# Optimization experiments

Measured on AMD Instinct MI355X. Metric: run time of the kernel, lower is better.

The kernel has to match this reference:

```python
import jax, jax.numpy as jnp
import numpy as np
import math

D_MODEL = 2048
NUM_HEADS = 16
HEAD_DIM = D_MODEL // NUM_HEADS  # 128
B, S = 2, 2048


def setup_inputs() -> dict:
    key = jax.random.key(0)
    ks = jax.random.split(key, 11)
    s_in = 1.0 / math.sqrt(D_MODEL)
    return {
        "query": jax.random.normal(ks[0], (B, S, D_MODEL), dtype=jnp.float32),
        "key": jax.random.normal(ks[1], (B, S, D_MODEL), dtype=jnp.float32),
        "value": jax.random.normal(ks[2], (B, S, D_MODEL), dtype=jnp.float32),
        "Wq": jax.random.normal(ks[3], (D_MODEL, D_MODEL), dtype=jnp.float32) * s_in,
        "bq": jnp.zeros((D_MODEL,), dtype=jnp.float32),
        "Wk": jax.random.normal(ks[4], (D_MODEL, HEAD_DIM), dtype=jnp.float32) * s_in,
        "bk": jnp.zeros((HEAD_DIM,), dtype=jnp.float32),
        "Wv": jax.random.normal(ks[5], (D_MODEL, HEAD_DIM), dtype=jnp.float32) * s_in,
        "bv": jnp.zeros((HEAD_DIM,), dtype=jnp.float32),
        "Wo": jax.random.normal(ks[6], (D_MODEL, D_MODEL), dtype=jnp.float32) * s_in,
        "bo": jnp.zeros((D_MODEL,), dtype=jnp.float32),
    }


def reference(query, key, value, Wq, bq, Wk, bk, Wv, bv, Wo, bo):
    b, s, d_model = query.shape
    h, d = NUM_HEADS, HEAD_DIM
    # Projections: Q has h heads, K/V have a single shared head (MQA)
    Q = (query @ Wq + bq).reshape(b, s, h, d).transpose(0, 2, 1, 3)  # [b,h,s,d]
    K = key @ Wk + bk      # [b,s,d]
    V = value @ Wv + bv    # [b,s,d]
    scale = 1.0 / math.sqrt(d)
    # broadcast single K head over all h query heads
    scores = jnp.einsum('bhqd,bkd->bhqk', Q, K) * scale  # [b,h,s,s]
    weights = jax.nn.softmax(scores, axis=-1)
    attn = jnp.einsum('bhqk,bkd->bhqd', weights, V)      # [b,h,s,d]
    attn = attn.transpose(0, 2, 1, 3).reshape(b, s, d_model)
    return attn @ Wo + bo
```

## Files before the change

kernel.cpp:

```cpp
#include <hip/hip_runtime.h>


typedef unsigned short u16;
typedef __attribute__((ext_vector_type(8))) short bf16x8;
typedef __attribute__((ext_vector_type(4))) short bf16x4;
typedef __attribute__((ext_vector_type(4))) float f32x4;

#define D_MODEL 2048
#define SEQ     2048
#define NH      16
#define HD      128
#define BK      32

__device__ __forceinline__ u16 f2bf(float f){
  union { float f; unsigned u; } v; v.f = f;
  unsigned r = (v.u + 0x7FFFu + ((v.u >> 16) & 1u)) >> 16;
  return (u16)r;
}

#if __has_builtin(__builtin_amdgcn_cvt_pk_bf16_f32)
__device__ __forceinline__ unsigned pack2bf(float a, float b){
  auto v = __builtin_amdgcn_cvt_pk_bf16_f32(a, b);
  unsigned u; __builtin_memcpy(&u, &v, 4); return u;
}
#else
__device__ __forceinline__ unsigned pack2bf(float a, float b){
  return (unsigned)f2bf(a) | ((unsigned)f2bf(b) << 16);
}
#endif

__device__ __forceinline__ void gll16(const void* g, void* l){
  __builtin_amdgcn_global_load_lds(
      (const __attribute__((address_space(1))) void*)g,
      (__attribute__((address_space(3))) void*)l, 16, 0, 0);
}

__global__ __launch_bounds__(256) void convert3_kernel(
    const float4* __restrict__ a, const float4* __restrict__ b, const float4* __restrict__ c,
    ushort4* __restrict__ oa, ushort4* __restrict__ ob, ushort4* __restrict__ oc){
  int i = blockIdx.x*256 + threadIdx.x;
  float4 va = a[i], vb = b[i], vc = c[i];
  ushort4 ra, rb, rc;
  ra.x=f2bf(va.x); ra.y=f2bf(va.y); ra.z=f2bf(va.z); ra.w=f2bf(va.w);
  rb.x=f2bf(vb.x); rb.y=f2bf(vb.y); rb.z=f2bf(vb.z); rb.w=f2bf(vb.w);
  rc.x=f2bf(vc.x); rc.y=f2bf(vc.y); rc.z=f2bf(vc.z); rc.w=f2bf(vc.w);
  oa[i]=ra; ob[i]=rb; oc[i]=rc;
}

__global__ __launch_bounds__(256) void transpose_all(
    const float* __restrict__ Wq, const float* __restrict__ Wo,
    const float* __restrict__ Wk, const float* __restrict__ Wv,
    u16* __restrict__ WqT, u16* __restrict__ WoT,
    u16* __restrict__ WkT, u16* __restrict__ WvT){
  __shared__ float tt[32][33];
  int id = blockIdx.x;
  const float* in; u16* outp; int C, bx, by;
  if (id < 4096)      { in=Wq; outp=WqT; C=2048; bx=id&63;        by=id>>6; }
  else if (id < 8192) { id-=4096; in=Wo; outp=WoT; C=2048; bx=id&63; by=id>>6; }
  else if (id < 8448) { id-=8192; in=Wk; outp=WkT; C=128;  bx=id&3;  by=id>>2; }
  else                { id-=8448; in=Wv; outp=WvT; C=128;  bx=id&3;  by=id>>2; }
  const int R = 2048;
  int c0 = bx*32, r0 = by*32;
  int tx = threadIdx.x & 31, ty = threadIdx.x >> 5;
  #pragma unroll
  for (int k=0;k<4;k++) tt[ty+k*8][tx] = in[(size_t)(r0+ty+k*8)*C + c0+tx];
  __syncthreads();
  #pragma unroll
  for (int k=0;k<4;k++) outp[(size_t)(c0+ty+k*8)*R + r0+tx] = f2bf(tt[tx][ty+k*8]);
}

__device__ __forceinline__ void gemm_core_db(
    const u16* __restrict__ A, const u16* __restrict__ BT,
    int lda, int ldb, int m0, int n0, int kbeg, int kend,
    u16* As, u16* Bs, f32x4 acc[4][4])
{
  const int t = threadIdx.x;
  const int w = t >> 6, l = t & 63;
  const int wr = w >> 1, wc = w & 1;
  const int c16 = l & 15, q = l >> 4;
  const int srow = l >> 2;
  const int sc   = ((l & 3) ^ ((l >> 3) & 3)) * 8;

  int aoff[4], boff[4];
  #pragma unroll
  for (int mt=0;mt<4;mt++){
    int row = wr*64 + mt*16 + c16;
    aoff[mt] = row*BK + ((q ^ ((row>>1)&3))*8);
  }
  #pragma unroll
  for (int nt=0;nt<4;nt++){
    int row = wc*64 + nt*16 + c16;
    boff[nt] = row*BK + ((q ^ ((row>>1)&3))*8);
  }

  auto issue = [&](int k0, int buf){
    u16* Ad = As + buf*4096;
    u16* Bd = Bs + buf*4096;
    #pragma unroll
    for (int half=0; half<2; half++){
      int r = half*64 + w*16 + srow;
      gll16(A  + (size_t)(m0+r)*lda + k0 + sc, Ad + (half*64 + w*16)*BK);
      gll16(BT + (size_t)(n0+r)*ldb + k0 + sc, Bd + (half*64 + w*16)*BK);
    }
  };

  const int n = (kend - kbeg) / BK;
  issue(kbeg, 0);
  for (int i = 0; i < n; i++){
    __syncthreads();
    if (i+1 < n) issue(kbeg + (i+1)*BK, (i+1)&1);
    const u16* Ab = As + (i&1)*4096;
    const u16* Bb = Bs + (i&1)*4096;
    bf16x8 af[4], bfr[4];
    #pragma unroll
    for (int mt=0;mt<4;mt++) af[mt]  = *(const bf16x8*)(Ab + aoff[mt]);
    #pragma unroll
    for (int nt=0;nt<4;nt++) bfr[nt] = *(const bf16x8*)(Bb + boff[nt]);
    #pragma unroll
    for (int mt=0;mt<4;mt++)
      #pragma unroll
      for (int nt=0;nt<4;nt++)
        acc[mt][nt] = __builtin_amdgcn_mfma_f32_16x16x32_bf16(af[mt], bfr[nt], acc[mt][nt], 0,0,0);
  }
}

__global__ __launch_bounds__(256) void proj_kernel(
    const u16* __restrict__ qb, const u16* __restrict__ kb, const u16* __restrict__ vb,
    const u16* __restrict__ WqT, const u16* __restrict__ WkT, const u16* __restrict__ WvT,
    const float* __restrict__ bq, u16* __restrict__ Qp, float* __restrict__ part)
{
  __shared__ u16 As[2*4096], Bs[2*4096];
  f32x4 acc[4][4];
  f32x4 z = {0.f,0.f,0.f,0.f};
  #pragma unroll
  for (int i=0;i<4;i++) for (int j=0;j<4;j++) acc[i][j] = z;
  const int t = threadIdx.x, w = t>>6, l = t&63, wr = w>>1, wc = w&1, c16 = l&15, q = l>>4;
  int id = blockIdx.x;
  if (id < 512){
    int m0 = (id & 31)*128, n0 = (id >> 5)*128;
    gemm_core_db(qb, WqT, 2048, 2048, m0, n0, 0, 2048, As, Bs, acc);
    #pragma unroll
    for (int mt=0;mt<4;mt++)
      #pragma unroll
      for (int nt=0;nt<4;nt++){
        int col = n0 + wc*64 + nt*16 + c16;
        float bv = bq[col];
        #pragma unroll
        for (int r=0;r<4;r++){
          int row = m0 + wr*64 + mt*16 + q*4 + r;
          Qp[(size_t)row*D_MODEL + col] = f2bf(acc[mt][nt][r] + bv);
        }
      }
  } else {
    int kvid = id - 512;
    int zi = kvid & 3, nb = (kvid >> 2) & 1, mi = kvid >> 3;
    const u16* Am = nb ? vb  : kb;
    const u16* Bm = nb ? WvT : WkT;
    gemm_core_db(Am, Bm, 2048, 2048, mi*128, 0, zi*512, zi*512+512, As, Bs, acc);
    float* dst = part + (size_t)(zi*2 + nb)*524288;
    #pragma unroll
    for (int mt=0;mt<4;mt++)
      #pragma unroll
      for (int nt=0;nt<4;nt++){
        int col = wc*64 + nt*16 + c16;
        #pragma unroll
        for (int r=0;r<4;r++){
          int row = mi*128 + wr*64 + mt*16 + q*4 + r;
          dst[(size_t)row*128 + col] = acc[mt][nt][r];
        }
      }
  }
}

__global__ __launch_bounds__(256) void oproj_kernel(
    const u16* __restrict__ A, const u16* __restrict__ BT, const float* __restrict__ bias,
    float* __restrict__ C)
{
  __shared__ u16 As[2*4096], Bs[2*4096];
  f32x4 acc[4][4];
  f32x4 z = {0.f,0.f,0.f,0.f};
  #pragma unroll
  for (int i=0;i<4;i++) for (int j=0;j<4;j++) acc[i][j] = z;
  int m0 = blockIdx.x*128, n0 = blockIdx.y*128;
  gemm_core_db(A, BT, 2048, 2048, m0, n0, 0, 2048, As, Bs, acc);
  const int t = threadIdx.x, w = t>>6, l = t&63, wr = w>>1, wc = w&1, c16 = l&15, q = l>>4;
  #pragma unroll
  for (int mt=0;mt<4;mt++)
    #pragma unroll
    for (int nt=0;nt<4;nt++){
      int col = n0 + wc*64 + nt*16 + c16;
      float bv = bias[col];
      #pragma unroll
      for (int r=0;r<4;r++){
        int row = m0 + wr*64 + mt*16 + q*4 + r;
        C[(size_t)row*D_MODEL + col] = acc[mt][nt][r] + bv;
      }
    }
}

__global__ __launch_bounds__(256) void kv_reduce_kernel(
    const float* __restrict__ part, const float* __restrict__ bk, const float* __restrict__ bv,
    u16* __restrict__ Kp, u16* __restrict__ VpT){
  int idx = blockIdx.x*256 + threadIdx.x;
  int d = idx & 127, sg = idx >> 7;
  float ka = 0.f, va = 0.f;
  #pragma unroll
  for (int zi=0; zi<4; zi++){
    ka += part[(size_t)(zi*2+0)*524288 + idx];
    va += part[(size_t)(zi*2+1)*524288 + idx];
  }
  Kp[idx] = f2bf(ka + bk[d]);
  int b = sg >> 11, sl = sg & 2047;
  VpT[(size_t)b*262144 + (size_t)d*2048 + sl] = f2bf(va + bv[d]);
}

__global__ __launch_bounds__(512, 2) void attn_kernel(
    const u16* __restrict__ Qp, const u16* __restrict__ Kp,
    const u16* __restrict__ VpT, u16* __restrict__ attnb){
  __shared__ u16 lds[65536];
  const int t = threadIdx.x;
  const int w = t >> 6, l = t & 63;
  const int c16 = l & 15, q = l >> 4;

  const int qt = blockIdx.x;
  const int bh = blockIdx.y;
  const int b = bh >> 4, h = bh & 15;

  const u16* Qbase = Qp  + ((size_t)(b*SEQ + qt*256 + w*32))*D_MODEL + h*HD;
  const u16* Kbase = Kp  + (size_t)(b*SEQ)*HD;
  const u16* Vbase = VpT + (size_t)b*HD*SEQ;

  const int sr = w*4 + (l >> 4);
  #pragma unroll
  for (int j=0;j<4;j++){
    int r = j*32 + sr;
    int g = (l & 15) ^ (r & 15);
    gll16(Kbase + (size_t)r*HD + g*8, lds + j*4096 + w*512);
  }
  #pragma unroll
  for (int j=0;j<4;j++){
    int d = j*32 + sr;
    int g = (l & 15) ^ (d & 15);
    gll16(Vbase + (size_t)d*SEQ + g*8, lds + 32768 + j*4096 + w*512);
  }
  bf16x8 qf[2][4];
  #pragma unroll
  for (int qs=0;qs<2;qs++)
    #pragma unroll
    for (int kk=0;kk<4;kk++)
      qf[qs][kk] = *(const bf16x8*)(Qbase + (size_t)(qs*16 + c16)*D_MODEL + (kk*4 + q)*8);
  __syncthreads();

  f32x4 o[2][8];
  f32x4 z4 = {0.f,0.f,0.f,0.f};
  #pragma unroll
  for (int qs=0;qs<2;qs++) for (int dt=0;dt<8;dt++) o[qs][dt] = z4;
  float mrow[2] = {-1e30f, -1e30f};
  float lrow[2] = {0.f, 0.f};
  const float cs = 0.08838834764831845f * 1.4426950408889634f;

  for (int kt = 0; kt < 16; kt++){
    const int p = kt & 1;
    if (kt < 15){
      u16* Kd = lds + (p^1)*16384;
      u16* Vd = lds + 32768 + (p^1)*16384;
      #pragma unroll
      for (int j=0;j<4;j++){
        int r = j*32 + sr;
        int g = (l & 15) ^ (r & 15);
        gll16(Kbase + (size_t)((kt+1)*128 + r)*HD + g*8, Kd + j*4096 + w*512);
      }
      #pragma unroll
      for (int j=0;j<4;j++){
        int d = j*32 + sr;
        int g = (l & 15) ^ (d & 15);
        gll16(Vbase + (size_t)d*SEQ + (kt+1)*128 + g*8, Vd + j*4096 + w*512);
      }
    }
    const u16* Ks = lds + p*16384;
    const u16* Vs = lds + 32768 + p*16384;

    f32x4 s[2][8];
    #pragma unroll
    for (int qs=0;qs<2;qs++) for (int kt8=0;kt8<8;kt8++) s[qs][kt8] = z4;
    __builtin_amdgcn_s_setprio(1);
    #pragma unroll
    for (int kt8=0; kt8<8; kt8++){
      #pragma unroll
      for (int kk=0;kk<4;kk++){
        int ch = kk*4 + q;
        bf16x8 kf = *(const bf16x8*)(Ks + (kt8*16 + c16)*128 + ((ch ^ c16) & 15)*8);
        s[0][kt8] = __builtin_amdgcn_mfma_f32_16x16x32_bf16(kf, qf[0][kk], s[0][kt8], 0,0,0);
        s[1][kt8] = __builtin_amdgcn_mfma_f32_16x16x32_bf16(kf, qf[1][kk], s[1][kt8], 0,0,0);
      }
    }
    __builtin_amdgcn_s_setprio(0);

    float alpha[2];
    #pragma unroll
    for (int qs=0; qs<2; qs++){
      float x[8];
      #pragma unroll
      for (int kt8=0;kt8<8;kt8++)
        x[kt8] = fmaxf(fmaxf(s[qs][kt8][0],s[qs][kt8][1]), fmaxf(s[qs][kt8][2],s[qs][kt8][3]));
      float vmax = fmaxf(fmaxf(fmaxf(x[0],x[1]),fmaxf(x[2],x[3])),
                         fmaxf(fmaxf(x[4],x[5]),fmaxf(x[6],x[7])));
      vmax = fmaxf(vmax, __shfl_xor(vmax, 16));
      vmax = fmaxf(vmax, __shfl_xor(vmax, 32));
      float mnew = fmaxf(mrow[qs], vmax);
      alpha[qs] = exp2f((mrow[qs] - mnew)*cs);
      float mc = mnew*cs;
      float rs[8];
      #pragma unroll
      for (int kt8=0;kt8<8;kt8++){
        float p0 = exp2f(__builtin_fmaf(s[qs][kt8][0], cs, -mc));
        float p1 = exp2f(__builtin_fmaf(s[qs][kt8][1], cs, -mc));
        float p2 = exp2f(__builtin_fmaf(s[qs][kt8][2], cs, -mc));
        float p3 = exp2f(__builtin_fmaf(s[qs][kt8][3], cs, -mc));
        s[qs][kt8][0]=p0; s[qs][kt8][1]=p1; s[qs][kt8][2]=p2; s[qs][kt8][3]=p3;
        rs[kt8] = (p0+p1)+(p2+p3);
      }
      float rsum = ((rs[0]+rs[1])+(rs[2]+rs[3])) + ((rs[4]+rs[5])+(rs[6]+rs[7]));
      rsum += __shfl_xor(rsum, 16);
      rsum += __shfl_xor(rsum, 32);
      lrow[qs] = lrow[qs]*alpha[qs] + rsum;
      mrow[qs] = mnew;
    }

    unsigned long long allone = __ballot(alpha[0] == 1.f && alpha[1] == 1.f);
    if (allone != ~0ull){
      #pragma unroll
      for (int qs=0;qs<2;qs++)
        #pragma unroll
        for (int dt=0;dt<8;dt++)
          #pragma unroll
          for (int r=0;r<4;r++) o[qs][dt][r] *= alpha[qs];
    }

    union PU { unsigned u[4]; bf16x8 v; } P32[2][4];
    #pragma unroll
    for (int qs=0;qs<2;qs++)
      #pragma unroll
      for (int kb=0;kb<4;kb++){
        P32[qs][kb].u[0] = pack2bf(s[qs][2*kb][0],   s[qs][2*kb][1]);
        P32[qs][kb].u[1] = pack2bf(s[qs][2*kb][2],   s[qs][2*kb][3]);
        P32[qs][kb].u[2] = pack2bf(s[qs][2*kb+1][0], s[qs][2*kb+1][1]);
        P32[qs][kb].u[3] = pack2bf(s[qs][2*kb+1][2], s[qs][2*kb+1][3]);
      }

    __builtin_amdgcn_s_setprio(1);
    #pragma unroll
    for (int kb=0; kb<4; kb++){
      int ca = 4*kb + (q>>1);
      int cb = ca + 2;
      #pragma unroll
      for (int dt=0; dt<8; dt++){
        int d = dt*16 + c16;
        union VU { bf16x4 h[2]; bf16x8 v; } vf;
        vf.h[0] = *(const bf16x4*)(Vs + d*128 + ((ca ^ c16) & 15)*8 + (q&1)*4);
        vf.h[1] = *(const bf16x4*)(Vs + d*128 + ((cb ^ c16) & 15)*8 + (q&1)*4);
        o[0][dt] = __builtin_amdgcn_mfma_f32_16x16x32_bf16(vf.v, P32[0][kb].v, o[0][dt], 0,0,0);
        o[1][dt] = __builtin_amdgcn_mfma_f32_16x16x32_bf16(vf.v, P32[1][kb].v, o[1][dt], 0,0,0);
      }
    }
    __builtin_amdgcn_s_setprio(0);
    __syncthreads();
  }

  #pragma unroll
  for (int qs=0;qs<2;qs++){
    float inv = 1.f / lrow[qs];
    int qrow = qt*256 + w*32 + qs*16 + c16;
    u16* dst = attnb + ((size_t)(b*SEQ) + qrow)*D_MODEL + h*HD + q*4;
    #pragma unroll
    for (int dt=0;dt<8;dt++){
      ushort4 pk;
      pk.x = f2bf(o[qs][dt][0]*inv);
      pk.y = f2bf(o[qs][dt][1]*inv);
      pk.z = f2bf(o[qs][dt][2]*inv);
      pk.w = f2bf(o[qs][dt][3]*inv);
      *(ushort4*)(dst + dt*16) = pk;
    }
  }
}

extern "C" void kernel_launch(void* const* d_in, const int* in_sizes, int n_in,
                              void* d_out, int out_size, void* d_ws, size_t ws_size,
                              hipStream_t stream) {
  (void)in_sizes; (void)n_in; (void)out_size; (void)ws_size;
  const float* query = (const float*)d_in[0];
  const float* key   = (const float*)d_in[1];
  const float* value = (const float*)d_in[2];
  const float* Wq    = (const float*)d_in[3];
  const float* bq    = (const float*)d_in[4];
  const float* Wk    = (const float*)d_in[5];
  const float* bk    = (const float*)d_in[6];
  const float* Wv    = (const float*)d_in[7];
  const float* bv    = (const float*)d_in[8];
  const float* Wo    = (const float*)d_in[9];
  const float* bo    = (const float*)d_in[10];
  float* out = (float*)d_out;

  char* W = (char*)d_ws;
  u16*  qb     = (u16*) (W + 0);
  u16*  kb     = (u16*) (W + 16777216);
  u16*  vb     = (u16*) (W + 33554432);
  u16*  WqT    = (u16*) (W + 50331648);
  u16*  WoT    = (u16*) (W + 58720256);
  u16*  WkT    = (u16*) (W + 67108864);
  u16*  WvT    = (u16*) (W + 67633152);
  u16*  Qp     = (u16*) (W + 68157440);
  u16*  Kp     = (u16*) (W + 84934656);
  u16*  VpT    = (u16*) (W + 85983232);
  u16*  attnb  = (u16*) (W + 87031808);
  float* kvpart= (float*)(W + 103809024);

  convert3_kernel<<<8192, 256, 0, stream>>>(
      (const float4*)query, (const float4*)key, (const float4*)value,
      (ushort4*)qb, (ushort4*)kb, (ushort4*)vb);
  transpose_all<<<8704, 256, 0, stream>>>(Wq, Wo, Wk, Wv, WqT, WoT, WkT, WvT);
  proj_kernel<<<768, 256, 0, stream>>>(qb, kb, vb, WqT, WkT, WvT, bq, Qp, kvpart);
  kv_reduce_kernel<<<2048, 256, 0, stream>>>(kvpart, bk, bv, Kp, VpT);
  attn_kernel<<<dim3(8,32), 512, 0, stream>>>(Qp, Kp, VpT, attnb);
  oproj_kernel<<<dim3(32,16), 256, 0, stream>>>(attnb, WoT, bo, out);
}
```

Baseline: 411.8 us.

## Split softmax into half-tiles with lazy max rescaling threshold

Splits each 128-key tile into two 64-key halves, each with its own max, exp, pack and PV MFMA phase. This lets softmax math for one half interleave with matrix work for the other. It also adds a lazy rescale: the running max and the output accumulator are updated only when some row's new max exceeds the old one by more than 8 in log2 units. Otherwise exponentials are computed against the stale max, which skips most rescale multiplies but risks larger intermediate values.

```diff
diff --git a/kernel.cpp b/kernel.cpp
--- a/kernel.cpp
+++ b/kernel.cpp
@@ -281,84 +281,175 @@
     const u16* Vs = lds + 32768 + p*16384;
 
     f32x4 s[2][8];
-    #pragma unroll
-    for (int qs=0;qs<2;qs++) for (int kt8=0;kt8<8;kt8++) s[qs][kt8] = z4;
+    union PU { unsigned u[4]; bf16x8 v; } P32[2][4];
+
     __builtin_amdgcn_s_setprio(1);
     #pragma unroll
-    for (int kt8=0; kt8<8; kt8++){
-      #pragma unroll
-      for (int kk=0;kk<4;kk++){
+    for (int kt8=0; kt8<4; kt8++){
+      {
+        bf16x8 kf = *(const bf16x8*)(Ks + (kt8*16 + c16)*128 + ((q ^ c16) & 15)*8);
+        s[0][kt8] = __builtin_amdgcn_mfma_f32_16x16x32_bf16(kf, qf[0][0], z4, 0,0,0);
+        s[1][kt8] = __builtin_amdgcn_mfma_f32_16x16x32_bf16(kf, qf[1][0], z4, 0,0,0);
+      }
+      #pragma unroll
+      for (int kk=1;kk<4;kk++){
         int ch = kk*4 + q;
         bf16x8 kf = *(const bf16x8*)(Ks + (kt8*16 + c16)*128 + ((ch ^ c16) & 15)*8);
         s[0][kt8] = __builtin_amdgcn_mfma_f32_16x16x32_bf16(kf, qf[0][kk], s[0][kt8], 0,0,0);
         s[1][kt8] = __builtin_amdgcn_mfma_f32_16x16x32_bf16(kf, qf[1][kk], s[1][kt8], 0,0,0);
       }
     }
+    #pragma unroll
+    for (int kt8=4; kt8<8; kt8++){
+      {
+        bf16x8 kf = *(const bf16x8*)(Ks + (kt8*16 + c16)*128 + ((q ^ c16) & 15)*8);
+        s[0][kt8] = __builtin_amdgcn_mfma_f32_16x16x32_bf16(kf, qf[0][0], z4, 0,0,0);
+        s[1][kt8] = __builtin_amdgcn_mfma_f32_16x16x32_bf16(kf, qf[1][0], z4, 0,0,0);
+      }
+      #pragma unroll
+      for (int kk=1;kk<4;kk++){
+        int ch = kk*4 + q;
+        bf16x8 kf = *(const bf16x8*)(Ks + (kt8*16 + c16)*128 + ((ch ^ c16) & 15)*8);
+        s[0][kt8] = __builtin_amdgcn_mfma_f32_16x16x32_bf16(kf, qf[0][kk], s[0][kt8], 0,0,0);
+        s[1][kt8] = __builtin_amdgcn_mfma_f32_16x16x32_bf16(kf, qf[1][kk], s[1][kt8], 0,0,0);
+      }
+    }
     __builtin_amdgcn_s_setprio(0);
 
-    float alpha[2];
-    #pragma unroll
-    for (int qs=0; qs<2; qs++){
-      float x[8];
-      #pragma unroll
-      for (int kt8=0;kt8<8;kt8++)
-        x[kt8] = fmaxf(fmaxf(s[qs][kt8][0],s[qs][kt8][1]), fmaxf(s[qs][kt8][2],s[qs][kt8][3]));
-      float vmax = fmaxf(fmaxf(fmaxf(x[0],x[1]),fmaxf(x[2],x[3])),
-                         fmaxf(fmaxf(x[4],x[5]),fmaxf(x[6],x[7])));
-      vmax = fmaxf(vmax, __shfl_xor(vmax, 16));
-      vmax = fmaxf(vmax, __shfl_xor(vmax, 32));
-      float mnew = fmaxf(mrow[qs], vmax);
-      alpha[qs] = exp2f((mrow[qs] - mnew)*cs);
-      float mc = mnew*cs;
-      float rs[8];
-      #pragma unroll
-      for (int kt8=0;kt8<8;kt8++){
-        float p0 = exp2f(__builtin_fmaf(s[qs][kt8][0], cs, -mc));
-        float p1 = exp2f(__builtin_fmaf(s[qs][kt8][1], cs, -mc));
-        float p2 = exp2f(__builtin_fmaf(s[qs][kt8][2], cs, -mc));
-        float p3 = exp2f(__builtin_fmaf(s[qs][kt8][3], cs, -mc));
-        s[qs][kt8][0]=p0; s[qs][kt8][1]=p1; s[qs][kt8][2]=p2; s[qs][kt8][3]=p3;
-        rs[kt8] = (p0+p1)+(p2+p3);
-      }
-      float rsum = ((rs[0]+rs[1])+(rs[2]+rs[3])) + ((rs[4]+rs[5])+(rs[6]+rs[7]));
-      rsum += __shfl_xor(rsum, 16);
-      rsum += __shfl_xor(rsum, 32);
-      lrow[qs] = lrow[qs]*alpha[qs] + rsum;
-      mrow[qs] = mnew;
-    }
-
-    unsigned long long allone = __ballot(alpha[0] == 1.f && alpha[1] == 1.f);
-    if (allone != ~0ull){
-      #pragma unroll
-      for (int qs=0;qs<2;qs++)
+    {
+      float vmax[2];
+      #pragma unroll
+      for (int qs=0; qs<2; qs++){
+        float x0 = fmaxf(fmaxf(s[qs][0][0],s[qs][0][1]), fmaxf(s[qs][0][2],s[qs][0][3]));
+        float x1 = fmaxf(fmaxf(s[qs][1][0],s[qs][1][1]), fmaxf(s[qs][1][2],s[qs][1][3]));
+        float x2 = fmaxf(fmaxf(s[qs][2][0],s[qs][2][1]), fmaxf(s[qs][2][2],s[qs][2][3]));
+        float x3 = fmaxf(fmaxf(s[qs][3][0],s[qs][3][1]), fmaxf(s[qs][3][2],s[qs][3][3]));
+        float vm = fmaxf(fmaxf(x0,x1), fmaxf(x2,x3));
+        vm = fmaxf(vm, __shfl_xor(vm, 16));
+        vm = fmaxf(vm, __shfl_xor(vm, 32));
+        vmax[qs] = vm;
+      }
+      bool upd = ((vmax[0]-mrow[0])*cs > 8.f) || ((vmax[1]-mrow[1])*cs > 8.f);
+      if (__any(upd)){
         #pragma unroll
-        for (int dt=0;dt<8;dt++)
+        for (int qs=0; qs<2; qs++){
+          float mnew = fmaxf(mrow[qs], vmax[qs]);
+          float a = exp2f((mrow[qs]-mnew)*cs);
+          mrow[qs] = mnew; lrow[qs] *= a;
           #pragma unroll
-          for (int r=0;r<4;r++) o[qs][dt][r] *= alpha[qs];
-    }
-
-    union PU { unsigned u[4]; bf16x8 v; } P32[2][4];
-    #pragma unroll
-    for (int qs=0;qs<2;qs++)
-      #pragma unroll
-      for (int kb=0;kb<4;kb++){
-        P32[qs][kb].u[0] = pack2bf(s[qs][2*kb][0],   s[qs][2*kb][1]);
-        P32[qs][kb].u[1] = pack2bf(s[qs][2*kb][2],   s[qs][2*kb][3]);
-        P32[qs][kb].u[2] = pack2bf(s[qs][2*kb+1][0], s[qs][2*kb+1][1]);
-        P32[qs][kb].u[3] = pack2bf(s[qs][2*kb+1][2], s[qs][2*kb+1][3]);
-      }
+          for (int dt=0;dt<8;dt++)
+            #pragma unroll
+            for (int r=0;r<4;r++) o[qs][dt][r] *= a;
+        }
+      }
+      #pragma unroll
+      for (int qs=0; qs<2; qs++){
+        float mc = mrow[qs]*cs;
+        float rsum = 0.f;
+        #pragma unroll
+        for (int kt8=0;kt8<4;kt8++){
+          float p0 = exp2f(__builtin_fmaf(s[qs][kt8][0], cs, -mc));
+          float p1 = exp2f(__builtin_fmaf(s[qs][kt8][1], cs, -mc));
+          float p2 = exp2f(__builtin_fmaf(s[qs][kt8][2], cs, -mc));
+          float p3 = exp2f(__builtin_fmaf(s[qs][kt8][3], cs, -mc));
+          s[qs][kt8][0]=p0; s[qs][kt8][1]=p1; s[qs][kt8][2]=p2; s[qs][kt8][3]=p3;
+          rsum += (p0+p1)+(p2+p3);
+        }
+        rsum += __shfl_xor(rsum, 16);
+        rsum += __shfl_xor(rsum, 32);
+        lrow[qs] += rsum;
+        P32[qs][0].u[0] = pack2bf(s[qs][0][0], s[qs][0][1]);
+        P32[qs][0].u[1] = pack2bf(s[qs][0][2], s[qs][0][3]);
+        P32[qs][0].u[2] = pack2bf(s[qs][1][0], s[qs][1][1]);
+        P32[qs][0].u[3] = pack2bf(s[qs][1][2], s[qs][1][3]);
+        P32[qs][1].u[0] = pack2bf(s[qs][2][0], s[qs][2][1]);
+        P32[qs][1].u[1] = pack2bf(s[qs][2][2], s[qs][2][3]);
+        P32[qs][1].u[2] = pack2bf(s[qs][3][0], s[qs][3][1]);
+        P32[qs][1].u[3] = pack2bf(s[qs][3][2], s[qs][3][3]);
+      }
+    }
 
     __builtin_amdgcn_s_setprio(1);
     #pragma unroll
-    for (int kb=0; kb<4; kb++){
+    for (int kb=0; kb<2; kb++){
       int ca = 4*kb + (q>>1);
       int cb = ca + 2;
       #pragma unroll
       for (int dt=0; dt<8; dt++){
         int d = dt*16 + c16;
-        union VU { bf16x4 h[2]; bf16x8 v; } vf;
-        vf.h[0] = *(const bf16x4*)(Vs + d*128 + ((ca ^ c16) & 15)*8 + (q&1)*4);
-        vf.h[1] = *(const bf16x4*)(Vs + d*128 + ((cb ^ c16) & 15)*8 + (q&1)*4);
+        union VU { bf16x4 hh[2]; bf16x8 v; } vf;
+        vf.hh[0] = *(const bf16x4*)(Vs + d*128 + ((ca ^ c16) & 15)*8 + (q&1)*4);
+        vf.hh[1] = *(const bf16x4*)(Vs + d*128 + ((cb ^ c16) & 15)*8 + (q&1)*4);
+        o[0][dt] = __builtin_amdgcn_mfma_f32_16x16x32_bf16(vf.v, P32[0][kb].v, o[0][dt], 0,0,0);
+        o[1][dt] = __builtin_amdgcn_mfma_f32_16x16x32_bf16(vf.v, P32[1][kb].v, o[1][dt], 0,0,0);
+      }
+    }
+    __builtin_amdgcn_s_setprio(0);
+
+    {
+      float vmax[2];
+      #pragma unroll
+      for (int qs=0; qs<2; qs++){
+        float x0 = fmaxf(fmaxf(s[qs][4][0],s[qs][4][1]), fmaxf(s[qs][4][2],s[qs][4][3]));
+        float x1 = fmaxf(fmaxf(s[qs][5][0],s[qs][5][1]), fmaxf(s[qs][5][2],s[qs][5][3]));
+        float x2 = fmaxf(fmaxf(s[qs][6][0],s[qs][6][1]), fmaxf(s[qs][6][2],s[qs][6][3]));
+        float x3 = fmaxf(fmaxf(s[qs][7][0],s[qs][7][1]), fmaxf(s[qs][7][2],s[qs][7][3]));
+        float vm = fmaxf(fmaxf(x0,x1), fmaxf(x2,x3));
+        vm = fmaxf(vm, __shfl_xor(vm, 16));
+        vm = fmaxf(vm, __shfl_xor(vm, 32));
+        vmax[qs] = vm;
+      }
+      bool upd = ((vmax[0]-mrow[0])*cs > 8.f) || ((vmax[1]-mrow[1])*cs > 8.f);
+      if (__any(upd)){
+        #pragma unroll
+        for (int qs=0; qs<2; qs++){
+          float mnew = fmaxf(mrow[qs], vmax[qs]);
+          float a = exp2f((mrow[qs]-mnew)*cs);
+          mrow[qs] = mnew; lrow[qs] *= a;
+          #pragma unroll
+          for (int dt=0;dt<8;dt++)
+            #pragma unroll
+            for (int r=0;r<4;r++) o[qs][dt][r] *= a;
+        }
+      }
+      #pragma unroll
+      for (int qs=0; qs<2; qs++){
+        float mc = mrow[qs]*cs;
+        float rsum = 0.f;
+        #pragma unroll
+        for (int kt8=4;kt8<8;kt8++){
+          float p0 = exp2f(__builtin_fmaf(s[qs][kt8][0], cs, -mc));
+          float p1 = exp2f(__builtin_fmaf(s[qs][kt8][1], cs, -mc));
+          float p2 = exp2f(__builtin_fmaf(s[qs][kt8][2], cs, -mc));
+          float p3 = exp2f(__builtin_fmaf(s[qs][kt8][3], cs, -mc));
+          s[qs][kt8][0]=p0; s[qs][kt8][1]=p1; s[qs][kt8][2]=p2; s[qs][kt8][3]=p3;
+          rsum += (p0+p1)+(p2+p3);
+        }
+        rsum += __shfl_xor(rsum, 16);
+        rsum += __shfl_xor(rsum, 32);
+        lrow[qs] += rsum;
+        P32[qs][2].u[0] = pack2bf(s[qs][4][0], s[qs][4][1]);
+        P32[qs][2].u[1] = pack2bf(s[qs][4][2], s[qs][4][3]);
+        P32[qs][2].u[2] = pack2bf(s[qs][5][0], s[qs][5][1]);
+        P32[qs][2].u[3] = pack2bf(s[qs][5][2], s[qs][5][3]);
+        P32[qs][3].u[0] = pack2bf(s[qs][6][0], s[qs][6][1]);
+        P32[qs][3].u[1] = pack2bf(s[qs][6][2], s[qs][6][3]);
+        P32[qs][3].u[2] = pack2bf(s[qs][7][0], s[qs][7][1]);
+        P32[qs][3].u[3] = pack2bf(s[qs][7][2], s[qs][7][3]);
+      }
+    }
+
+    __builtin_amdgcn_s_setprio(1);
+    #pragma unroll
+    for (int kb=2; kb<4; kb++){
+      int ca = 4*kb + (q>>1);
+      int cb = ca + 2;
+      #pragma unroll
+      for (int dt=0; dt<8; dt++){
+        int d = dt*16 + c16;
+        union VU { bf16x4 hh[2]; bf16x8 v; } vf;
+        vf.hh[0] = *(const bf16x4*)(Vs + d*128 + ((ca ^ c16) & 15)*8 + (q&1)*4);
+        vf.hh[1] = *(const bf16x4*)(Vs + d*128 + ((cb ^ c16) & 15)*8 + (q&1)*4);
         o[0][dt] = __builtin_amdgcn_mfma_f32_16x16x32_bf16(vf.v, P32[0][kb].v, o[0][dt], 0,0,0);
         o[1][dt] = __builtin_amdgcn_mfma_f32_16x16x32_bf16(vf.v, P32[1][kb].v, o[1][dt], 0,0,0);
       }
```

After: 413.0 us. About the same (+0.3%).
